# Optimization experiments

Measured on AMD Instinct MI355X. Metric: run time of the kernel, lower is better.

## Reference

```python
import jax, jax.numpy as jnp
import numpy as np

N = 100000   # num entities
D = 128      # embed_dim
S = 8192     # num sparse nodes
P = 16       # paths per node (padded; invalid paths fully masked)
K = 16       # max endpoints per path (padded via mask)
H = D // 2   # MLP hidden


def setup_inputs() -> dict:
    key = jax.random.key(0)
    ks = jax.random.split(key, 6)
    entity_embeds = jax.random.normal(ks[0], (N, D), dtype=jnp.float32)
    sparse_ids = jnp.arange(S, dtype=jnp.int32)  # distinct sparse node ids
    endpoint_ids = jax.random.randint(ks[1], (S, P, K), 0, N, dtype=jnp.int32)
    endpoint_mask = jax.random.randint(ks[2], (S, P, K), 0, 2).astype(bool)
    W1 = jax.random.normal(ks[3], (D, H), dtype=jnp.float32) * (1.0 / np.sqrt(D))
    b1 = jnp.zeros((H,), dtype=jnp.float32)
    W2 = jax.random.normal(ks[4], (H, 1), dtype=jnp.float32) * (1.0 / np.sqrt(H))
    b2 = jnp.zeros((1,), dtype=jnp.float32)
    return {"entity_embeds": entity_embeds, "W1": W1, "b1": b1, "W2": W2,
            "b2": b2, "sparse_ids": sparse_ids, "endpoint_ids": endpoint_ids,
            "endpoint_mask": endpoint_mask}


def reference(entity_embeds, W1, b1, W2, b2, sparse_ids, endpoint_ids, endpoint_mask):
    # Gather endpoint embeddings reached by each (sparse node, path): [S,P,K,D]
    gathered = entity_embeds[endpoint_ids]
    m = endpoint_mask.astype(entity_embeds.dtype)[..., None]
    cnt = endpoint_mask.sum(-1)                                   # [S,P] endpoints per path
    agg = (gathered * m).sum(2) / jnp.maximum(cnt, 1)[..., None]  # masked mean [S,P,D]
    # path_weight_net: Linear -> ReLU -> Linear -> Sigmoid (scalar weight per path)
    h = jax.nn.relu(agg @ W1 + b1)                                # [S,P,H]
    w = jax.nn.sigmoid(h @ W2 + b2)                               # [S,P,1]
    valid = cnt > 0                                               # path had endpoints
    feat = jnp.where(valid[..., None], w * agg, 0.0)              # [S,P,D]
    nv = valid.sum(1)                                             # valid paths per node [S]
    node_feat = feat.sum(1) / jnp.maximum(nv, 1)[:, None]         # mean over valid paths
    node_feat = jnp.where((nv > 0)[:, None], node_feat, 0.0)
    # scatter per-sparse-node aggregate into [N,D] (others stay zero)
    remote = jnp.zeros_like(entity_embeds).at[sparse_ids].set(node_feat)
    return remote
```

## Files before the change

kernel.cpp:

```cpp
#include <hip/hip_runtime.h>
#include <hip/hip_bf16.h>

#define S_NODES 8192
#define P_PATHS 16
#define K_EP    16
#define D_DIM   128
#define H_DIM   64

typedef __bf16 bf16x8_t __attribute__((ext_vector_type(8)));
typedef float  f32x4_t  __attribute__((ext_vector_type(4)));

#define AGGF_STRIDE  132
#define AGGBF_STRIDE 136

__global__ __launch_bounds__(256)
void prep_fused_kernel(const float* __restrict__ ent, const float* __restrict__ W1,
                       __bf16* __restrict__ entbf, __bf16* __restrict__ w1t,
                       float4* __restrict__ out4, int n4, int o4)
{
    const int i = blockIdx.x * 256 + threadIdx.x;
    if (i < n4) {
        float4 v = ((const float4*)ent)[i];
        union { __bf16 h[4]; uint2 u; } pk;
        pk.h[0] = (__bf16)v.x; pk.h[1] = (__bf16)v.y;
        pk.h[2] = (__bf16)v.z; pk.h[3] = (__bf16)v.w;
        ((uint2*)entbf)[i] = pk.u;
    }
    if (i < 32)
        ((uint2*)entbf)[n4 + i] = make_uint2(0u, 0u);
    if (i < o4) out4[i] = make_float4(0.f, 0.f, 0.f, 0.f);
    if (i < D_DIM * H_DIM) {
        const int n = i >> 7, d = i & 127;
        w1t[i] = (__bf16)W1[d * H_DIM + n];
    }
}

__global__ __launch_bounds__(256)
void prep_w1_kernel(const float* __restrict__ W1, __bf16* __restrict__ w1t)
{
    const int idx = blockIdx.x * 256 + threadIdx.x;
    const int n = idx >> 7, d = idx & 127;
    w1t[idx] = (__bf16)W1[d * H_DIM + n];
}

__device__ __forceinline__ void acc_row(float4& lo, float4& hi, uint4 r)
{
    lo.x += __uint_as_float(r.x << 16); lo.y += __uint_as_float(r.x & 0xffff0000u);
    lo.z += __uint_as_float(r.y << 16); lo.w += __uint_as_float(r.y & 0xffff0000u);
    hi.x += __uint_as_float(r.z << 16); hi.y += __uint_as_float(r.z & 0xffff0000u);
    hi.z += __uint_as_float(r.w << 16); hi.w += __uint_as_float(r.w & 0xffff0000u);
}

template<bool USE_BF16>
__global__ __launch_bounds__(256, 5)
void PathGuidedAggregator_kernel(const float*  __restrict__ ent,
                                 const __bf16* __restrict__ entbf,
                                 const float*  __restrict__ b1,
                                 const float*  __restrict__ W2,
                                 const float*  __restrict__ b2,
                                 const int*    __restrict__ sids,
                                 const int*    __restrict__ eids,
                                 const void*   __restrict__ emask,
                                 const __bf16* __restrict__ w1t,
                                 float*        __restrict__ out,
                                 int nent)
{
    __shared__ float  aggf [P_PATHS][AGGF_STRIDE];
    __shared__ __bf16 aggbf[P_PATHS][AGGBF_STRIDE];
    __shared__ int    cnts[P_PATHS];
    __shared__ int    comp[4][4][K_EP];

    const int s    = blockIdx.x;
    const int tid  = threadIdx.x;
    const int wave = tid >> 6;
    const int lane = tid & 63;

    const unsigned int* mw = (const unsigned int*)emask;
    unsigned int probe = mw[lane];
    const bool floatMask = (__ballot(probe == 0x3F800000u) != 0ULL);
    const bool byteMask  = !floatMask && (__ballot(probe > 1u) != 0ULL);

    const int base = (s * P_PATHS + wave * 4) * K_EP;
    const int idv  = eids[base + lane];
    int mk;
    if (floatMask)     mk = (((const float*)emask)[base + lane] != 0.0f);
    else if (byteMask) mk = ((const unsigned char*)emask)[base + lane];
    else               mk = ((const int*)emask)[base + lane];
    const unsigned long long bits_all = __ballot(mk != 0);

    const int k16  = lane & 15;
    const int pgrp = lane >> 4;

    const unsigned int bits_p = (unsigned int)((bits_all >> (16 * pgrp)) & 0xFFFFu);
    comp[wave][pgrp][k16] = USE_BF16 ? nent : 0;
    if (mk) comp[wave][pgrp][__popc(bits_p & ((1u << k16) - 1u))] = idv;
    if (lane < 4) cnts[wave * 4 + lane] = __popc((unsigned int)((bits_all >> (16 * lane)) & 0xFFFFu));

    const int c0 = __popc((unsigned int)( bits_all        & 0xFFFFu));
    const int c1 = __popc((unsigned int)((bits_all >> 16) & 0xFFFFu));
    const int c2 = __popc((unsigned int)((bits_all >> 32) & 0xFFFFu));
    const int c3 = __popc((unsigned int)((bits_all >> 48) & 0xFFFFu));

    const int q   = lane >> 4;
    const int c16 = lane & 15;

    if constexpr (USE_BF16) {
        const uint4* __restrict__ entb = (const uint4*)entbf;
        float4 l0 = {0,0,0,0}, h0 = l0, l1 = l0, h1 = l0, l2 = l0, h2 = l0, l3 = l0, h3 = l0;

        uint4 r0 = entb[(size_t)comp[wave][q    ][q] * 16 + c16];
        uint4 r1 = entb[(size_t)comp[wave][q ^ 1][q] * 16 + c16];
        uint4 r2 = entb[(size_t)comp[wave][q ^ 2][q] * 16 + c16];
        uint4 r3 = entb[(size_t)comp[wave][q ^ 3][q] * 16 + c16];
        #pragma unroll
        for (int u = 0; u < 4; ++u) {
            uint4 n0, n1, n2, n3;
            if (u < 3) {
                const int slot = q + 4 * (u + 1);
                n0 = entb[(size_t)comp[wave][q    ][slot] * 16 + c16];
                n1 = entb[(size_t)comp[wave][q ^ 1][slot] * 16 + c16];
                n2 = entb[(size_t)comp[wave][q ^ 2][slot] * 16 + c16];
                n3 = entb[(size_t)comp[wave][q ^ 3][slot] * 16 + c16];
            }
            acc_row(l0, h0, r0);
            acc_row(l1, h1, r1);
            acc_row(l2, h2, r2);
            acc_row(l3, h3, r3);
            if (u < 3) { r0 = n0; r1 = n1; r2 = n2; r3 = n3; }
        }
        l0.x += __shfl_xor(l1.x, 16); l0.y += __shfl_xor(l1.y, 16);
        l0.z += __shfl_xor(l1.z, 16); l0.w += __shfl_xor(l1.w, 16);
        h0.x += __shfl_xor(h1.x, 16); h0.y += __shfl_xor(h1.y, 16);
        h0.z += __shfl_xor(h1.z, 16); h0.w += __shfl_xor(h1.w, 16);
        l2.x += __shfl_xor(l3.x, 16); l2.y += __shfl_xor(l3.y, 16);
        l2.z += __shfl_xor(l3.z, 16); l2.w += __shfl_xor(l3.w, 16);
        h2.x += __shfl_xor(h3.x, 16); h2.y += __shfl_xor(h3.y, 16);
        h2.z += __shfl_xor(h3.z, 16); h2.w += __shfl_xor(h3.w, 16);
        l0.x += __shfl_xor(l2.x, 32); l0.y += __shfl_xor(l2.y, 32);
        l0.z += __shfl_xor(l2.z, 32); l0.w += __shfl_xor(l2.w, 32);
        h0.x += __shfl_xor(h2.x, 32); h0.y += __shfl_xor(h2.y, 32);
        h0.z += __shfl_xor(h2.z, 32); h0.w += __shfl_xor(h2.w, 32);

        const int   cq   = __popc((unsigned int)((bits_all >> (16 * q)) & 0xFFFFu));
        const float invq = 1.0f / (float)(cq > 1 ? cq : 1);
        l0.x *= invq; l0.y *= invq; l0.z *= invq; l0.w *= invq;
        h0.x *= invq; h0.y *= invq; h0.z *= invq; h0.w *= invq;
        const int pw = wave * 4 + q;
        *(float4*)&aggf[pw][c16 * 8]     = l0;
        *(float4*)&aggf[pw][c16 * 8 + 4] = h0;
        union { __bf16 h[8]; uint4 u4; } pk;
        pk.h[0] = (__bf16)l0.x; pk.h[1] = (__bf16)l0.y; pk.h[2] = (__bf16)l0.z; pk.h[3] = (__bf16)l0.w;
        pk.h[4] = (__bf16)h0.x; pk.h[5] = (__bf16)h0.y; pk.h[6] = (__bf16)h0.z; pk.h[7] = (__bf16)h0.w;
        *(uint4*)&aggbf[pw][c16 * 8] = pk.u4;
    } else {
        const int half = lane >> 5;
        const int col  = lane & 31;
        const float4* __restrict__ entc = (const float4*)ent + col;
        float4 acc0 = {0.f,0.f,0.f,0.f}, acc1 = acc0, acc2 = acc0, acc3 = acc0;
        #pragma unroll
        for (int u = 0; u < 8; ++u) {
            const int slot = 2 * u + half;
            const int id0 = comp[wave][0][slot];
            const int id1 = comp[wave][1][slot];
            const int id2 = comp[wave][2][slot];
            const int id3 = comp[wave][3][slot];
            if (slot < c0) { float4 v = entc[(size_t)id0 << 5]; acc0.x += v.x; acc0.y += v.y; acc0.z += v.z; acc0.w += v.w; }
            if (slot < c1) { float4 v = entc[(size_t)id1 << 5]; acc1.x += v.x; acc1.y += v.y; acc1.z += v.z; acc1.w += v.w; }
            if (slot < c2) { float4 v = entc[(size_t)id2 << 5]; acc2.x += v.x; acc2.y += v.y; acc2.z += v.z; acc2.w += v.w; }
            if (slot < c3) { float4 v = entc[(size_t)id3 << 5]; acc3.x += v.x; acc3.y += v.y; acc3.z += v.z; acc3.w += v.w; }
        }
        #pragma unroll
        for (int i = 0; i < 4; ++i) {
            float4 a = (i == 0) ? acc0 : (i == 1) ? acc1 : (i == 2) ? acc2 : acc3;
            const int cnt = (i == 0) ? c0 : (i == 1) ? c1 : (i == 2) ? c2 : c3;
            a.x += __shfl_xor(a.x, 32); a.y += __shfl_xor(a.y, 32);
            a.z += __shfl_xor(a.z, 32); a.w += __shfl_xor(a.w, 32);
            const float inv = 1.0f / (float)(cnt > 1 ? cnt : 1);
            a.x *= inv; a.y *= inv; a.z *= inv; a.w *= inv;
            if (half == 0) {
                const int p = wave * 4 + i;
                *(float4*)&aggf[p][col * 4] = a;
                union { __bf16 h[4]; uint2 u2; } pk;
                pk.h[0] = (__bf16)a.x; pk.h[1] = (__bf16)a.y;
                pk.h[2] = (__bf16)a.z; pk.h[3] = (__bf16)a.w;
                *(uint2*)&aggbf[p][col * 4] = pk.u2;
            }
        }
    }
    __syncthreads();

    if (wave != 0) return;

    const int m    = lane & 15;
    const int quad = lane >> 4;

    bf16x8_t afr[4];
    #pragma unroll
    for (int st = 0; st < 4; ++st)
        afr[st] = *(const bf16x8_t*)&aggbf[m][st * 32 + quad * 8];

    float xp[4] = {0.f, 0.f, 0.f, 0.f};
    #pragma unroll
    for (int t = 0; t < 4; ++t) {
        const int n = t * 16 + m;
        const float b1v = b1[n];
        f32x4_t acc = {b1v, b1v, b1v, b1v};
        const __bf16* bp = w1t + n * D_DIM + quad * 8;
        #pragma unroll
        for (int st = 0; st < 4; ++st) {
            bf16x8_t bfr = *(const bf16x8_t*)(bp + st * 32);
            acc = __builtin_amdgcn_mfma_f32_16x16x32_bf16(afr[st], bfr, acc, 0, 0, 0);
        }
        const float w2v = W2[n];
        #pragma unroll
        for (int r = 0; r < 4; ++r) {
            float h = acc[r] > 0.f ? acc[r] : 0.f;
            xp[r] += h * w2v;
        }
    }
    #pragma unroll
    for (int off = 1; off < 16; off <<= 1) {
        #pragma unroll
        for (int r = 0; r < 4; ++r) xp[r] += __shfl_xor(xp[r], off);
    }

    int myc[4]; int localv = 0;
    #pragma unroll
    for (int r = 0; r < 4; ++r) { myc[r] = cnts[quad * 4 + r]; localv += (myc[r] > 0); }
    int nv = localv + __shfl_xor(localv, 16);
    nv += __shfl_xor(nv, 32);
    const float invnv = 1.0f / (float)(nv > 1 ? nv : 1);
    const float b2v = b2[0];

    float wv[4];
    #pragma unroll
    for (int r = 0; r < 4; ++r) {
        float x = xp[r] + b2v;
        float w = 1.0f / (1.0f + __expf(-x));
        wv[r] = (myc[r] > 0) ? w * invnv : 0.f;
    }

    float fx = 0.f, fy = 0.f;
    #pragma unroll
    for (int p = 0; p < P_PATHS; ++p) {
        float wp = __shfl(wv[p & 3], (p >> 2) << 4);
        float2 a = *(const float2*)&aggf[p][2 * lane];
        fx += wp * a.x; fy += wp * a.y;
    }
    const int row = sids[s];
    *(float2*)&out[(size_t)row * D_DIM + 2 * lane] = make_float2(fx, fy);
}

extern "C" void kernel_launch(void* const* d_in, const int* in_sizes, int n_in,
                              void* d_out, int out_size, void* d_ws, size_t ws_size,
                              hipStream_t stream)
{
    const float* ent  = (const float*)d_in[0];
    const float* W1   = (const float*)d_in[1];
    const float* b1   = (const float*)d_in[2];
    const float* W2   = (const float*)d_in[3];
    const float* b2   = (const float*)d_in[4];
    const int*   sids = (const int*)d_in[5];
    const int*   eids = (const int*)d_in[6];
    const void*  emsk = (const void*)d_in[7];
    float* out = (float*)d_out;

    const int ND   = in_sizes[0];
    const int nent = ND / D_DIM;
    __bf16* w1t_ws = (__bf16*)d_ws;
    __bf16* entbf  = (__bf16*)((char*)d_ws + 16384);
    const bool useBf16 = (ws_size >= 16384 + ((size_t)ND + D_DIM) * 2)
                         && ((ND & 3) == 0) && ((out_size & 3) == 0);

    if (useBf16) {
        const int n4 = ND >> 2, o4 = out_size >> 2;
        const int mx = n4 > o4 ? n4 : o4;
        prep_fused_kernel<<<(mx + 255) / 256, 256, 0, stream>>>(ent, W1, entbf, w1t_ws,
                                                                (float4*)out, n4, o4);
        PathGuidedAggregator_kernel<true><<<S_NODES, 256, 0, stream>>>(
            ent, (const __bf16*)entbf, b1, W2, b2, sids, eids, emsk,
            (const __bf16*)w1t_ws, out, nent);
    } else {
        hipMemsetAsync(d_out, 0, (size_t)out_size * sizeof(float), stream);
        prep_w1_kernel<<<32, 256, 0, stream>>>(W1, w1t_ws);
        PathGuidedAggregator_kernel<false><<<S_NODES, 256, 0, stream>>>(
            ent, (const __bf16*)entbf, b1, W2, b2, sids, eids, emsk,
            (const __bf16*)w1t_ws, out, nent);
    }
}
```

Baseline: 163.4 us.

## Give each lane group one path and accumulate all 16 endpoints without shuffles

Changes the bf16 gather so each 16-lane group reads all 16 compacted endpoint rows of its own path, instead of interleaving the four paths across groups and combining partial sums with cross-lane shuffles. An 8-deep register ring prefetch replaces the 4-wide double buffer, and accumulation uses vector float4 adds. This removes 24 shuffle-add steps per path and raises memory-level parallelism per lane, at the cost of more live registers (8 uint4 buffers) under a launch bound of 5 waves.

```diff
diff --git a/kernel.cpp b/kernel.cpp
--- a/kernel.cpp
+++ b/kernel.cpp
@@ -43,12 +43,14 @@
     w1t[idx] = (__bf16)W1[d * H_DIM + n];
 }
 
-__device__ __forceinline__ void acc_row(float4& lo, float4& hi, uint4 r)
-{
-    lo.x += __uint_as_float(r.x << 16); lo.y += __uint_as_float(r.x & 0xffff0000u);
-    lo.z += __uint_as_float(r.y << 16); lo.w += __uint_as_float(r.y & 0xffff0000u);
-    hi.x += __uint_as_float(r.z << 16); hi.y += __uint_as_float(r.z & 0xffff0000u);
-    hi.z += __uint_as_float(r.w << 16); hi.w += __uint_as_float(r.w & 0xffff0000u);
+__device__ __forceinline__ void acc_unpack(f32x4_t& lo, f32x4_t& hi, uint4 r)
+{
+    f32x4_t a, b;
+    a[0] = __uint_as_float(r.x << 16); a[1] = __uint_as_float(r.x & 0xffff0000u);
+    a[2] = __uint_as_float(r.y << 16); a[3] = __uint_as_float(r.y & 0xffff0000u);
+    b[0] = __uint_as_float(r.z << 16); b[1] = __uint_as_float(r.z & 0xffff0000u);
+    b[2] = __uint_as_float(r.w << 16); b[3] = __uint_as_float(r.w & 0xffff0000u);
+    lo += a; hi += b;
 }
 
 template<bool USE_BF16>
@@ -106,51 +108,30 @@
 
     if constexpr (USE_BF16) {
         const uint4* __restrict__ entb = (const uint4*)entbf;
-        float4 l0 = {0,0,0,0}, h0 = l0, l1 = l0, h1 = l0, l2 = l0, h2 = l0, l3 = l0, h3 = l0;
-
-        uint4 r0 = entb[(size_t)comp[wave][q    ][q] * 16 + c16];
-        uint4 r1 = entb[(size_t)comp[wave][q ^ 1][q] * 16 + c16];
-        uint4 r2 = entb[(size_t)comp[wave][q ^ 2][q] * 16 + c16];
-        uint4 r3 = entb[(size_t)comp[wave][q ^ 3][q] * 16 + c16];
-        #pragma unroll
-        for (int u = 0; u < 4; ++u) {
-            uint4 n0, n1, n2, n3;
-            if (u < 3) {
-                const int slot = q + 4 * (u + 1);
-                n0 = entb[(size_t)comp[wave][q    ][slot] * 16 + c16];
-                n1 = entb[(size_t)comp[wave][q ^ 1][slot] * 16 + c16];
-                n2 = entb[(size_t)comp[wave][q ^ 2][slot] * 16 + c16];
-                n3 = entb[(size_t)comp[wave][q ^ 3][slot] * 16 + c16];
-            }
-            acc_row(l0, h0, r0);
-            acc_row(l1, h1, r1);
-            acc_row(l2, h2, r2);
-            acc_row(l3, h3, r3);
-            if (u < 3) { r0 = n0; r1 = n1; r2 = n2; r3 = n3; }
-        }
-        l0.x += __shfl_xor(l1.x, 16); l0.y += __shfl_xor(l1.y, 16);
-        l0.z += __shfl_xor(l1.z, 16); l0.w += __shfl_xor(l1.w, 16);
-        h0.x += __shfl_xor(h1.x, 16); h0.y += __shfl_xor(h1.y, 16);
-        h0.z += __shfl_xor(h1.z, 16); h0.w += __shfl_xor(h1.w, 16);
-        l2.x += __shfl_xor(l3.x, 16); l2.y += __shfl_xor(l3.y, 16);
-        l2.z += __shfl_xor(l3.z, 16); l2.w += __shfl_xor(l3.w, 16);
-        h2.x += __shfl_xor(h3.x, 16); h2.y += __shfl_xor(h3.y, 16);
-        h2.z += __shfl_xor(h3.z, 16); h2.w += __shfl_xor(h3.w, 16);
-        l0.x += __shfl_xor(l2.x, 32); l0.y += __shfl_xor(l2.y, 32);
-        l0.z += __shfl_xor(l2.z, 32); l0.w += __shfl_xor(l2.w, 32);
-        h0.x += __shfl_xor(h2.x, 32); h0.y += __shfl_xor(h2.y, 32);
-        h0.z += __shfl_xor(h2.z, 32); h0.w += __shfl_xor(h2.w, 32);
+        f32x4_t lo = {0.f, 0.f, 0.f, 0.f}, hi = lo;
+
+        uint4 rbuf[8];
+        #pragma unroll
+        for (int u = 0; u < 8; ++u)
+            rbuf[u] = entb[(size_t)comp[wave][q][u] * 16 + c16];
+
+        #pragma unroll
+        for (int u = 0; u < 16; ++u) {
+            uint4 r = rbuf[u & 7];
+            if (u < 8)
+                rbuf[u & 7] = entb[(size_t)comp[wave][q][u + 8] * 16 + c16];
+            acc_unpack(lo, hi, r);
+        }
 
         const int   cq   = __popc((unsigned int)((bits_all >> (16 * q)) & 0xFFFFu));
         const float invq = 1.0f / (float)(cq > 1 ? cq : 1);
-        l0.x *= invq; l0.y *= invq; l0.z *= invq; l0.w *= invq;
-        h0.x *= invq; h0.y *= invq; h0.z *= invq; h0.w *= invq;
+        lo *= invq; hi *= invq;
         const int pw = wave * 4 + q;
-        *(float4*)&aggf[pw][c16 * 8]     = l0;
-        *(float4*)&aggf[pw][c16 * 8 + 4] = h0;
+        *(float4*)&aggf[pw][c16 * 8]     = *(float4*)&lo;
+        *(float4*)&aggf[pw][c16 * 8 + 4] = *(float4*)&hi;
         union { __bf16 h[8]; uint4 u4; } pk;
-        pk.h[0] = (__bf16)l0.x; pk.h[1] = (__bf16)l0.y; pk.h[2] = (__bf16)l0.z; pk.h[3] = (__bf16)l0.w;
-        pk.h[4] = (__bf16)h0.x; pk.h[5] = (__bf16)h0.y; pk.h[6] = (__bf16)h0.z; pk.h[7] = (__bf16)h0.w;
+        pk.h[0] = (__bf16)lo[0]; pk.h[1] = (__bf16)lo[1]; pk.h[2] = (__bf16)lo[2]; pk.h[3] = (__bf16)lo[3];
+        pk.h[4] = (__bf16)hi[0]; pk.h[5] = (__bf16)hi[1]; pk.h[6] = (__bf16)hi[2]; pk.h[7] = (__bf16)hi[3];
         *(uint4*)&aggbf[pw][c16 * 8] = pk.u4;
     } else {
         const int half = lane >> 5;
```

New measurement: 166.8 us. +2.1%, slower.

## Process two sparse nodes per block so two waves run the MLP epilogue

Applied to the files above, without the earlier changes.

Each block now handles two sparse nodes. All four waves gather endpoint rows for both nodes in sequence, then waves 0 and 1 each run the MFMA path-weight MLP and the weighted reduction for one node. This halves the grid and the per-block launch and mask-probe overhead, and lets two waves share the epilogue instead of one. In exchange the gather phase of each block is serialised over two nodes and shared memory per block doubles, which may reduce occupancy.

```diff
diff --git a/kernel.cpp b/kernel.cpp
--- a/kernel.cpp
+++ b/kernel.cpp
@@ -6,6 +6,7 @@
 #define K_EP    16
 #define D_DIM   128
 #define H_DIM   64
+#define NODES_PER_BLK 2
 
 typedef __bf16 bf16x8_t __attribute__((ext_vector_type(8)));
 typedef float  f32x4_t  __attribute__((ext_vector_type(4)));
@@ -65,12 +66,12 @@
                                  float*        __restrict__ out,
                                  int nent)
 {
-    __shared__ float  aggf [P_PATHS][AGGF_STRIDE];
-    __shared__ __bf16 aggbf[P_PATHS][AGGBF_STRIDE];
-    __shared__ int    cnts[P_PATHS];
-    __shared__ int    comp[4][4][K_EP];
-
-    const int s    = blockIdx.x;
+    __shared__ float  aggf [NODES_PER_BLK][P_PATHS][AGGF_STRIDE];
+    __shared__ __bf16 aggbf[NODES_PER_BLK][P_PATHS][AGGBF_STRIDE];
+    __shared__ int    cnts[NODES_PER_BLK][P_PATHS];
+    __shared__ int    comp[NODES_PER_BLK][4][4][K_EP];
+
+    const int s0   = blockIdx.x * NODES_PER_BLK;
     const int tid  = threadIdx.x;
     const int wave = tid >> 6;
     const int lane = tid & 63;
@@ -80,116 +81,120 @@
     const bool floatMask = (__ballot(probe == 0x3F800000u) != 0ULL);
     const bool byteMask  = !floatMask && (__ballot(probe > 1u) != 0ULL);
 
-    const int base = (s * P_PATHS + wave * 4) * K_EP;
-    const int idv  = eids[base + lane];
-    int mk;
-    if (floatMask)     mk = (((const float*)emask)[base + lane] != 0.0f);
-    else if (byteMask) mk = ((const unsigned char*)emask)[base + lane];
-    else               mk = ((const int*)emask)[base + lane];
-    const unsigned long long bits_all = __ballot(mk != 0);
-
     const int k16  = lane & 15;
     const int pgrp = lane >> 4;
-
-    const unsigned int bits_p = (unsigned int)((bits_all >> (16 * pgrp)) & 0xFFFFu);
-    comp[wave][pgrp][k16] = USE_BF16 ? nent : 0;
-    if (mk) comp[wave][pgrp][__popc(bits_p & ((1u << k16) - 1u))] = idv;
-    if (lane < 4) cnts[wave * 4 + lane] = __popc((unsigned int)((bits_all >> (16 * lane)) & 0xFFFFu));
-
-    const int c0 = __popc((unsigned int)( bits_all        & 0xFFFFu));
-    const int c1 = __popc((unsigned int)((bits_all >> 16) & 0xFFFFu));
-    const int c2 = __popc((unsigned int)((bits_all >> 32) & 0xFFFFu));
-    const int c3 = __popc((unsigned int)((bits_all >> 48) & 0xFFFFu));
-
-    const int q   = lane >> 4;
-    const int c16 = lane & 15;
-
-    if constexpr (USE_BF16) {
-        const uint4* __restrict__ entb = (const uint4*)entbf;
-        float4 l0 = {0,0,0,0}, h0 = l0, l1 = l0, h1 = l0, l2 = l0, h2 = l0, l3 = l0, h3 = l0;
-
-        uint4 r0 = entb[(size_t)comp[wave][q    ][q] * 16 + c16];
-        uint4 r1 = entb[(size_t)comp[wave][q ^ 1][q] * 16 + c16];
-        uint4 r2 = entb[(size_t)comp[wave][q ^ 2][q] * 16 + c16];
-        uint4 r3 = entb[(size_t)comp[wave][q ^ 3][q] * 16 + c16];
-        #pragma unroll
-        for (int u = 0; u < 4; ++u) {
-            uint4 n0, n1, n2, n3;
-            if (u < 3) {
-                const int slot = q + 4 * (u + 1);
-                n0 = entb[(size_t)comp[wave][q    ][slot] * 16 + c16];
-                n1 = entb[(size_t)comp[wave][q ^ 1][slot] * 16 + c16];
-                n2 = entb[(size_t)comp[wave][q ^ 2][slot] * 16 + c16];
-                n3 = entb[(size_t)comp[wave][q ^ 3][slot] * 16 + c16];
+    const int q    = lane >> 4;
+    const int c16  = lane & 15;
+
+    for (int rnd = 0; rnd < NODES_PER_BLK; ++rnd) {
+        const int s = s0 + rnd;
+        const int base = (s * P_PATHS + wave * 4) * K_EP;
+        const int idv  = eids[base + lane];
+        int mk;
+        if (floatMask)     mk = (((const float*)emask)[base + lane] != 0.0f);
+        else if (byteMask) mk = ((const unsigned char*)emask)[base + lane];
+        else               mk = ((const int*)emask)[base + lane];
+        const unsigned long long bits_all = __ballot(mk != 0);
+
+        const unsigned int bits_p = (unsigned int)((bits_all >> (16 * pgrp)) & 0xFFFFu);
+        comp[rnd][wave][pgrp][k16] = USE_BF16 ? nent : 0;
+        if (mk) comp[rnd][wave][pgrp][__popc(bits_p & ((1u << k16) - 1u))] = idv;
+        if (lane < 4) cnts[rnd][wave * 4 + lane] =
+            __popc((unsigned int)((bits_all >> (16 * lane)) & 0xFFFFu));
+
+        const int c0 = __popc((unsigned int)( bits_all        & 0xFFFFu));
+        const int c1 = __popc((unsigned int)((bits_all >> 16) & 0xFFFFu));
+        const int c2 = __popc((unsigned int)((bits_all >> 32) & 0xFFFFu));
+        const int c3 = __popc((unsigned int)((bits_all >> 48) & 0xFFFFu));
+
+        if constexpr (USE_BF16) {
+            const uint4* __restrict__ entb = (const uint4*)entbf;
+            float4 l0 = {0,0,0,0}, h0 = l0, l1 = l0, h1 = l0, l2 = l0, h2 = l0, l3 = l0, h3 = l0;
+
+            uint4 r0 = entb[(size_t)comp[rnd][wave][q    ][q] * 16 + c16];
+            uint4 r1 = entb[(size_t)comp[rnd][wave][q ^ 1][q] * 16 + c16];
+            uint4 r2 = entb[(size_t)comp[rnd][wave][q ^ 2][q] * 16 + c16];
+            uint4 r3 = entb[(size_t)comp[rnd][wave][q ^ 3][q] * 16 + c16];
+            #pragma unroll
+            for (int u = 0; u < 4; ++u) {
+                uint4 n0, n1, n2, n3;
+                if (u < 3) {
+                    const int slot = q + 4 * (u + 1);
+                    n0 = entb[(size_t)comp[rnd][wave][q    ][slot] * 16 + c16];
+                    n1 = entb[(size_t)comp[rnd][wave][q ^ 1][slot] * 16 + c16];
+                    n2 = entb[(size_t)comp[rnd][wave][q ^ 2][slot] * 16 + c16];
+                    n3 = entb[(size_t)comp[rnd][wave][q ^ 3][slot] * 16 + c16];
+                }
+                acc_row(l0, h0, r0);
+                acc_row(l1, h1, r1);
+                acc_row(l2, h2, r2);
+                acc_row(l3, h3, r3);
+                if (u < 3) { r0 = n0; r1 = n1; r2 = n2; r3 = n3; }
             }
-            acc_row(l0, h0, r0);
-            acc_row(l1, h1, r1);
-            acc_row(l2, h2, r2);
-            acc_row(l3, h3, r3);
-            if (u < 3) { r0 = n0; r1 = n1; r2 = n2; r3 = n3; }
-        }
-        l0.x += __shfl_xor(l1.x, 16); l0.y += __shfl_xor(l1.y, 16);
-        l0.z += __shfl_xor(l1.z, 16); l0.w += __shfl_xor(l1.w, 16);
-        h0.x += __shfl_xor(h1.x, 16); h0.y += __shfl_xor(h1.y, 16);
-        h0.z += __shfl_xor(h1.z, 16); h0.w += __shfl_xor(h1.w, 16);
-        l2.x += __shfl_xor(l3.x, 16); l2.y += __shfl_xor(l3.y, 16);
-        l2.z += __shfl_xor(l3.z, 16); l2.w += __shfl_xor(l3.w, 16);
-        h2.x += __shfl_xor(h3.x, 16); h2.y += __shfl_xor(h3.y, 16);
-        h2.z += __shfl_xor(h3.z, 16); h2.w += __shfl_xor(h3.w, 16);
-        l0.x += __shfl_xor(l2.x, 32); l0.y += __shfl_xor(l2.y, 32);
-        l0.z += __shfl_xor(l2.z, 32); l0.w += __shfl_xor(l2.w, 32);
-        h0.x += __shfl_xor(h2.x, 32); h0.y += __shfl_xor(h2.y, 32);
-        h0.z += __shfl_xor(h2.z, 32); h0.w += __shfl_xor(h2.w, 32);
-
-        const int   cq   = __popc((unsigned int)((bits_all >> (16 * q)) & 0xFFFFu));
-        const float invq = 1.0f / (float)(cq > 1 ? cq : 1);
-        l0.x *= invq; l0.y *= invq; l0.z *= invq; l0.w *= invq;
-        h0.x *= invq; h0.y *= invq; h0.z *= invq; h0.w *= invq;
-        const int pw = wave * 4 + q;
-        *(float4*)&aggf[pw][c16 * 8]     = l0;
-        *(float4*)&aggf[pw][c16 * 8 + 4] = h0;
-        union { __bf16 h[8]; uint4 u4; } pk;
-        pk.h[0] = (__bf16)l0.x; pk.h[1] = (__bf16)l0.y; pk.h[2] = (__bf16)l0.z; pk.h[3] = (__bf16)l0.w;
-        pk.h[4] = (__bf16)h0.x; pk.h[5] = (__bf16)h0.y; pk.h[6] = (__bf16)h0.z; pk.h[7] = (__bf16)h0.w;
-        *(uint4*)&aggbf[pw][c16 * 8] = pk.u4;
-    } else {
-        const int half = lane >> 5;
-        const int col  = lane & 31;
-        const float4* __restrict__ entc = (const float4*)ent + col;
-        float4 acc0 = {0.f,0.f,0.f,0.f}, acc1 = acc0, acc2 = acc0, acc3 = acc0;
-        #pragma unroll
-        for (int u = 0; u < 8; ++u) {
-            const int slot = 2 * u + half;
-            const int id0 = comp[wave][0][slot];
-            const int id1 = comp[wave][1][slot];
-            const int id2 = comp[wave][2][slot];
-            const int id3 = comp[wave][3][slot];
-            if (slot < c0) { float4 v = entc[(size_t)id0 << 5]; acc0.x += v.x; acc0.y += v.y; acc0.z += v.z; acc0.w += v.w; }
-            if (slot < c1) { float4 v = entc[(size_t)id1 << 5]; acc1.x += v.x; acc1.y += v.y; acc1.z += v.z; acc1.w += v.w; }
-            if (slot < c2) { float4 v = entc[(size_t)id2 << 5]; acc2.x += v.x; acc2.y += v.y; acc2.z += v.z; acc2.w += v.w; }
-            if (slot < c3) { float4 v = entc[(size_t)id3 << 5]; acc3.x += v.x; acc3.y += v.y; acc3.z += v.z; acc3.w += v.w; }
-        }
-        #pragma unroll
-        for (int i = 0; i < 4; ++i) {
-            float4 a = (i == 0) ? acc0 : (i == 1) ? acc1 : (i == 2) ? acc2 : acc3;
-            const int cnt = (i == 0) ? c0 : (i == 1) ? c1 : (i == 2) ? c2 : c3;
-            a.x += __shfl_xor(a.x, 32); a.y += __shfl_xor(a.y, 32);
-            a.z += __shfl_xor(a.z, 32); a.w += __shfl_xor(a.w, 32);
-            const float inv = 1.0f / (float)(cnt > 1 ? cnt : 1);
-            a.x *= inv; a.y *= inv; a.z *= inv; a.w *= inv;
-            if (half == 0) {
-                const int p = wave * 4 + i;
-                *(float4*)&aggf[p][col * 4] = a;
-                union { __bf16 h[4]; uint2 u2; } pk;
-                pk.h[0] = (__bf16)a.x; pk.h[1] = (__bf16)a.y;
-                pk.h[2] = (__bf16)a.z; pk.h[3] = (__bf16)a.w;
-                *(uint2*)&aggbf[p][col * 4] = pk.u2;
+            l0.x += __shfl_xor(l1.x, 16); l0.y += __shfl_xor(l1.y, 16);
+            l0.z += __shfl_xor(l1.z, 16); l0.w += __shfl_xor(l1.w, 16);
+            h0.x += __shfl_xor(h1.x, 16); h0.y += __shfl_xor(h1.y, 16);
+            h0.z += __shfl_xor(h1.z, 16); h0.w += __shfl_xor(h1.w, 16);
+            l2.x += __shfl_xor(l3.x, 16); l2.y += __shfl_xor(l3.y, 16);
+            l2.z += __shfl_xor(l3.z, 16); l2.w += __shfl_xor(l3.w, 16);
+            h2.x += __shfl_xor(h3.x, 16); h2.y += __shfl_xor(h3.y, 16);
+            h2.z += __shfl_xor(h3.z, 16); h2.w += __shfl_xor(h3.w, 16);
+            l0.x += __shfl_xor(l2.x, 32); l0.y += __shfl_xor(l2.y, 32);
+            l0.z += __shfl_xor(l2.z, 32); l0.w += __shfl_xor(l2.w, 32);
+            h0.x += __shfl_xor(h2.x, 32); h0.y += __shfl_xor(h2.y, 32);
+            h0.z += __shfl_xor(h2.z, 32); h0.w += __shfl_xor(h2.w, 32);
+
+            const int   cq   = __popc((unsigned int)((bits_all >> (16 * q)) & 0xFFFFu));
+            const float invq = 1.0f / (float)(cq > 1 ? cq : 1);
+            l0.x *= invq; l0.y *= invq; l0.z *= invq; l0.w *= invq;
+            h0.x *= invq; h0.y *= invq; h0.z *= invq; h0.w *= invq;
+            const int pw = wave * 4 + q;
+            *(float4*)&aggf[rnd][pw][c16 * 8]     = l0;
+            *(float4*)&aggf[rnd][pw][c16 * 8 + 4] = h0;
+            union { __bf16 h[8]; uint4 u4; } pk;
+            pk.h[0] = (__bf16)l0.x; pk.h[1] = (__bf16)l0.y; pk.h[2] = (__bf16)l0.z; pk.h[3] = (__bf16)l0.w;
+            pk.h[4] = (__bf16)h0.x; pk.h[5] = (__bf16)h0.y; pk.h[6] = (__bf16)h0.z; pk.h[7] = (__bf16)h0.w;
+            *(uint4*)&aggbf[rnd][pw][c16 * 8] = pk.u4;
+        } else {
+            const int half = lane >> 5;
+            const int col  = lane & 31;
+            const float4* __restrict__ entc = (const float4*)ent + col;
+            float4 acc0 = {0.f,0.f,0.f,0.f}, acc1 = acc0, acc2 = acc0, acc3 = acc0;
+            #pragma unroll
+            for (int u = 0; u < 8; ++u) {
+                const int slot = 2 * u + half;
+                const int id0 = comp[rnd][wave][0][slot];
+                const int id1 = comp[rnd][wave][1][slot];
+                const int id2 = comp[rnd][wave][2][slot];
+                const int id3 = comp[rnd][wave][3][slot];
+                if (slot < c0) { float4 v = entc[(size_t)id0 << 5]; acc0.x += v.x; acc0.y += v.y; acc0.z += v.z; acc0.w += v.w; }
+                if (slot < c1) { float4 v = entc[(size_t)id1 << 5]; acc1.x += v.x; acc1.y += v.y; acc1.z += v.z; acc1.w += v.w; }
+                if (slot < c2) { float4 v = entc[(size_t)id2 << 5]; acc2.x += v.x; acc2.y += v.y; acc2.z += v.z; acc2.w += v.w; }
+                if (slot < c3) { float4 v = entc[(size_t)id3 << 5]; acc3.x += v.x; acc3.y += v.y; acc3.z += v.z; acc3.w += v.w; }
+            }
+            #pragma unroll
+            for (int i = 0; i < 4; ++i) {
+                float4 a = (i == 0) ? acc0 : (i == 1) ? acc1 : (i == 2) ? acc2 : acc3;
+                const int cnt = (i == 0) ? c0 : (i == 1) ? c1 : (i == 2) ? c2 : c3;
+                a.x += __shfl_xor(a.x, 32); a.y += __shfl_xor(a.y, 32);
+                a.z += __shfl_xor(a.z, 32); a.w += __shfl_xor(a.w, 32);
+                const float inv = 1.0f / (float)(cnt > 1 ? cnt : 1);
+                a.x *= inv; a.y *= inv; a.z *= inv; a.w *= inv;
+                if (half == 0) {
+                    const int p = wave * 4 + i;
+                    *(float4*)&aggf[rnd][p][col * 4] = a;
+                    union { __bf16 h[4]; uint2 u2; } pk;
+                    pk.h[0] = (__bf16)a.x; pk.h[1] = (__bf16)a.y;
+                    pk.h[2] = (__bf16)a.z; pk.h[3] = (__bf16)a.w;
+                    *(uint2*)&aggbf[rnd][p][col * 4] = pk.u2;
+                }
             }
         }
     }
     __syncthreads();
 
-    if (wave != 0) return;
+    if (wave >= NODES_PER_BLK) return;
+    const int node = wave;
 
     const int m    = lane & 15;
     const int quad = lane >> 4;
@@ -197,7 +202,7 @@
     bf16x8_t afr[4];
     #pragma unroll
     for (int st = 0; st < 4; ++st)
-        afr[st] = *(const bf16x8_t*)&aggbf[m][st * 32 + quad * 8];
+        afr[st] = *(const bf16x8_t*)&aggbf[node][m][st * 32 + quad * 8];
 
     float xp[4] = {0.f, 0.f, 0.f, 0.f};
     #pragma unroll
@@ -226,7 +231,7 @@
 
     int myc[4]; int localv = 0;
     #pragma unroll
-    for (int r = 0; r < 4; ++r) { myc[r] = cnts[quad * 4 + r]; localv += (myc[r] > 0); }
+    for (int r = 0; r < 4; ++r) { myc[r] = cnts[node][quad * 4 + r]; localv += (myc[r] > 0); }
     int nv = localv + __shfl_xor(localv, 16);
     nv += __shfl_xor(nv, 32);
     const float invnv = 1.0f / (float)(nv > 1 ? nv : 1);
@@ -244,10 +249,10 @@
     #pragma unroll
     for (int p = 0; p < P_PATHS; ++p) {
         float wp = __shfl(wv[p & 3], (p >> 2) << 4);
-        float2 a = *(const float2*)&aggf[p][2 * lane];
+        float2 a = *(const float2*)&aggf[node][p][2 * lane];
         fx += wp * a.x; fy += wp * a.y;
     }
-    const int row = sids[s];
+    const int row = sids[s0 + node];
     *(float2*)&out[(size_t)row * D_DIM + 2 * lane] = make_float2(fx, fy);
 }
 
@@ -277,13 +282,13 @@
         const int mx = n4 > o4 ? n4 : o4;
         prep_fused_kernel<<<(mx + 255) / 256, 256, 0, stream>>>(ent, W1, entbf, w1t_ws,
                                                                 (float4*)out, n4, o4);
-        PathGuidedAggregator_kernel<true><<<S_NODES, 256, 0, stream>>>(
+        PathGuidedAggregator_kernel<true><<<S_NODES / NODES_PER_BLK, 256, 0, stream>>>(
             ent, (const __bf16*)entbf, b1, W2, b2, sids, eids, emsk,
             (const __bf16*)w1t_ws, out, nent);
     } else {
         hipMemsetAsync(d_out, 0, (size_t)out_size * sizeof(float), stream);
         prep_w1_kernel<<<32, 256, 0, stream>>>(W1, w1t_ws);
-        PathGuidedAggregator_kernel<false><<<S_NODES, 256, 0, stream>>>(
+        PathGuidedAggregator_kernel<false><<<S_NODES / NODES_PER_BLK, 256, 0, stream>>>(
             ent, (const __bf16*)entbf, b1, W2, b2, sids, eids, emsk,
             (const __bf16*)w1t_ws, out, nent);
     }
```

Measured after the change: 169.3 us. 1.04x slower.
